# Kernel optimization log

Hardware: AMD Instinct MI355X
Metric: run time of the kernel (lower is better)

## Reference

```python
import jax, jax.numpy as jnp
import numpy as np

V, E, S, B, N = 100000, 300, 1024, 64, 5
H = [512, 256, 128]

def setup_inputs() -> dict:
    key = jax.random.key(0)
    ks = jax.random.split(key, 10)
    x = jax.random.randint(ks[0], (B, S), 0, V, dtype=jnp.int32)
    # lengths must be >= n for valid n-gram counts (original assumes this)
    lengths = jax.random.randint(ks[1], (B,), N, S + 1, dtype=jnp.int32)
    sc = lambda f: 1.0 / np.sqrt(f)
    table = jax.random.normal(ks[2], (V, E), dtype=jnp.float32)
    W_slide = jax.random.uniform(ks[3], (N * E, H[0]), jnp.float32, -sc(N * E), sc(N * E))
    b_slide = jax.random.uniform(ks[4], (H[0],), jnp.float32, -sc(N * E), sc(N * E))
    W1 = jax.random.uniform(ks[5], (H[0], H[1]), jnp.float32, -sc(H[0]), sc(H[0]))
    b1 = jax.random.uniform(ks[6], (H[1],), jnp.float32, -sc(H[0]), sc(H[0]))
    W2 = jax.random.uniform(ks[7], (H[1], H[2]), jnp.float32, -sc(H[1]), sc(H[1]))
    b2 = jax.random.uniform(ks[8], (H[2],), jnp.float32, -sc(H[1]), sc(H[1]))
    return {"x": x, "lengths": lengths, "table": table, "W_slide": W_slide,
            "b_slide": b_slide, "W1": W1, "b1": b1, "W2": W2, "b2": b2}

def reference(x, lengths, table, W_slide, b_slide, W1, b1, W2, b2):
    n = N
    Wn = S - (n - 1)  # number of sliding windows per sequence
    emb = table[x]  # [B, S, E]
    # gather sliding windows: [B, Wn, n, E] -> [B, Wn, n*E]
    idx = jnp.arange(Wn)[:, None] + jnp.arange(n)[None, :]
    win = emb[:, idx].reshape(B, Wn, n * E)
    h = win @ W_slide + b_slide              # [B, Wn, H0]
    h = jax.nn.relu(h @ W1 + b1)             # [B, Wn, H1]
    h = jax.nn.relu(h @ W2 + b2)             # [B, Wn, H2]
    # ragged mean over valid n-gram positions per sample
    valid = (lengths - (n - 1)).astype(h.dtype)           # [B]
    mask = (jnp.arange(Wn)[None, :] < (lengths - (n - 1))[:, None]).astype(h.dtype)
    pooled = jnp.einsum('bwh,bw->bh', h, mask) / valid[:, None]
    return pooled
```

## Files before the change

### kernel.cpp

```cpp
#include <hip/hip_runtime.h>

#define B_N    64
#define S_LEN  1024
#define EMB    300
#define EMB_P  304
#define NGRAM  5
#define WPAD   1024
#define MTOT   (B_N * WPAD)
#define K1P    1536
#define H0     512
#define H1D    256
#define H2D    128
#define NK1    (K1P / 32)
#define NSTEP1 (K1P / 64)

#define GATHER_BLOCKS ((MTOT * 38) / 256)
#define WPREP_THREADS (H0 * K1P + H1D * H0 + H2D * H1D)
#define WPREP_BLOCKS  ((WPREP_THREADS + 255) / 256)

typedef _Float16 half8 __attribute__((ext_vector_type(8)));
typedef float  floatx4 __attribute__((ext_vector_type(4)));

typedef const __attribute__((address_space(1))) void* gptr_t;
typedef __attribute__((address_space(3))) void* sptr_t;

__device__ __forceinline__ void gload16(const void* g, void* s) {
  __builtin_amdgcn_global_load_lds((gptr_t)g, (sptr_t)s, 16, 0, 0);
}

__global__ void prep_kernel(const int* __restrict__ x,
                            const int* __restrict__ lengths,
                            const float* __restrict__ table,
                            _Float16* __restrict__ emb,
                            float* __restrict__ out,
                            const float* __restrict__ Ws,
                            const float* __restrict__ W1,
                            const float* __restrict__ W2,
                            _Float16* __restrict__ Bf1,
                            _Float16* __restrict__ Bf2,
                            _Float16* __restrict__ Bf3,
                            int* __restrict__ meta) {
  __shared__ int sN[64], sP[65], sN6[64], sP6[65];
  const int bid = blockIdx.x;
  if (bid < GATHER_BLOCKS) {
    if (bid < 32) out[bid * 256 + threadIdx.x] = 0.0f;
    int tid = bid * 256 + threadIdx.x;
    int tok = tid / 38;
    int c   = tid - tok * 38;
    int valid = lengths[tok >> 10] - (NGRAM - 1);
    int limit = ((valid + 127) & ~127) + (NGRAM - 1);
    if ((tok & 1023) >= limit) return;
    int e = c << 3;
    const float* row = table + (size_t)x[tok] * EMB + e;
    float4 v0 = *(const float4*)row;
    float4 v1 = make_float4(0.0f, 0.0f, 0.0f, 0.0f);
    if (e + 4 < EMB) v1 = *(const float4*)(row + 4);
    union { half8 h8; _Float16 h[8]; } u;
    u.h[0] = (_Float16)v0.x; u.h[1] = (_Float16)v0.y;
    u.h[2] = (_Float16)v0.z; u.h[3] = (_Float16)v0.w;
    u.h[4] = (_Float16)v1.x; u.h[5] = (_Float16)v1.y;
    u.h[6] = (_Float16)v1.z; u.h[7] = (_Float16)v1.w;
    *(half8*)(emb + (size_t)tok * EMB_P + e) = u.h8;
  } else if (bid < GATHER_BLOCKS + WPREP_BLOCKS) {
    int tid = (bid - GATHER_BLOCKS) * 256 + threadIdx.x;
    const int NS = H0 * K1P;
    const int N1 = H1D * H0;
    const int N2 = H2D * H1D;
    if (tid < NS) {
      int n = tid & 511, k = tid >> 9;
      float v = 0.0f;
      if (k < NGRAM * EMB_P) {
        int tn = k / EMB_P, e = k - tn * EMB_P;
        if (e < EMB) v = Ws[(size_t)(tn * EMB + e) * H0 + n];
      }
      int idx = ((((n >> 4) * NK1 + (k >> 5)) << 6) + (((k >> 3) & 3) << 4) + (n & 15)) * 8 + (k & 7);
      Bf1[idx] = (_Float16)v;
    } else if (tid < NS + N1) {
      int t = tid - NS;
      int n = t & 255, k = t >> 8;
      float v = W1[(size_t)k * H1D + n];
      int idx = ((((n >> 4) * 16 + (k >> 5)) << 6) + (((k >> 3) & 3) << 4) + (n & 15)) * 8 + (k & 7);
      Bf2[idx] = (_Float16)v;
    } else if (tid < NS + N1 + N2) {
      int t = tid - (NS + N1);
      int n = t & 127, k = t >> 7;
      float v = W2[(size_t)k * H2D + n];
      int idx = ((((n >> 4) * 8 + (k >> 5)) << 6) + (((k >> 3) & 3) << 4) + (n & 15)) * 8 + (k & 7);
      Bf3[idx] = (_Float16)v;
    }
  } else {
    int t = threadIdx.x;
    if (t < 64) {
      int valid = lengths[t] - (NGRAM - 1);
      sN[t]  = (valid + 127) >> 7;
      sN6[t] = (valid + 63) >> 6;
    }
    __syncthreads();
    if (t == 0) {
      int s = 0, s6 = 0;
      for (int i = 0; i < 64; i++) {
        sP[i] = s;   s  += sN[i];
        sP6[i] = s6; s6 += sN6[i];
      }
      meta[0] = s; meta[1] = s6;
    }
    __syncthreads();
    if (t < 64) {
      int base = sP[t], n = sN[t];
      for (int i = 0; i < n; i++) meta[8 + base + i] = (t << 3) + i;
      int b6 = sP6[t], n6 = sN6[t];
      for (int i = 0; i < n6; i++) meta[520 + b6 + i] = (t << 4) + i;
    }
  }
}

__global__ __launch_bounds__(256, 2)
void gemm1(const _Float16* __restrict__ A, const _Float16* __restrict__ Bf,
           const float* __restrict__ bias, _Float16* __restrict__ Cf,
           const int* __restrict__ meta, int xcdBase) {
  __shared__ _Float16 sA[2][128 * 64];
  __shared__ _Float16 sB[2][128 * 64];

  const int nLive4 = meta[0] << 2;
  const int xcd = xcdBase + (blockIdx.x & 3), bi = blockIdx.x >> 2;
  const int q = nLive4 >> 3, r = nLive4 & 7;
  if (bi >= q + (xcd < r ? 1 : 0)) return;
  const int L = xcd * q + (xcd < r ? xcd : r) + bi;
  const int mt = meta[8 + (L >> 2)], nt = L & 3;

  const int tid  = threadIdx.x;
  const int wave = tid >> 6, lane = tid & 63;
  const int wr   = wave >> 1, wc = wave & 1;
  const int quad = lane >> 4, l16 = lane & 15;

  const long mBase = (long)mt << 7;
  const int  nBase = nt << 7;

  const int srow0  = (wave << 3) + (lane >> 3);
  const int schunk = lane & 7;
  const _Float16* aG[4];
  int sOffA[4];
#pragma unroll
  for (int p = 0; p < 4; p++) {
    int row = (p << 5) + srow0;
    int c   = schunk ^ (row & 7);
    aG[p]   = A + (mBase + row) * EMB_P + (c << 3);
    sOffA[p] = (row << 6) + (schunk << 3);
  }

  const _Float16* bSrc[4];
  int sOffB[4];
#pragma unroll
  for (int p = 0; p < 4; p++) {
    int idx   = (p << 8) + tid;
    int n16l  = idx >> 7;
    int s     = (idx >> 6) & 1;
    int lane_s = idx & 63;
    bSrc[p]  = Bf + (((size_t)((nBase >> 4) + n16l) * NK1 + s) << 9) + (lane_s << 3);
    sOffB[p] = idx << 3;
  }

  int aOff[2][4];
#pragma unroll
  for (int s = 0; s < 2; s++)
#pragma unroll
    for (int i = 0; i < 4; i++) {
      int rr   = (wr << 6) + (i << 4) + l16;
      int slot = ((s << 2) + quad) ^ (l16 & 7);
      aOff[s][i] = (rr << 6) + (slot << 3);
    }
  int bOff[2][4];
#pragma unroll
  for (int s = 0; s < 2; s++)
#pragma unroll
    for (int j = 0; j < 4; j++)
      bOff[s][j] = (((((wc << 2) + j) << 1) + s) << 9) + (lane << 3);

  floatx4 acc[4][4] = {};

#pragma unroll
  for (int p = 0; p < 4; p++) gload16(aG[p], &sA[0][sOffA[p]]);
#pragma unroll
  for (int p = 0; p < 4; p++) gload16(bSrc[p], &sB[0][sOffB[p]]);

#pragma unroll 2
  for (int kk = 0; kk < NSTEP1; kk++) {
    const int cur = kk & 1;
    __syncthreads();
    if (kk + 1 < NSTEP1) {
      const int koA = (kk + 1) << 6;
      const size_t koB = (size_t)(kk + 1) << 10;
#pragma unroll
      for (int p = 0; p < 4; p++) gload16(aG[p] + koA, &sA[cur ^ 1][sOffA[p]]);
#pragma unroll
      for (int p = 0; p < 4; p++) gload16(bSrc[p] + koB, &sB[cur ^ 1][sOffB[p]]);
    }
#pragma unroll
    for (int s = 0; s < 2; s++) {
      half8 aFr[4], bFr[4];
#pragma unroll
      for (int i = 0; i < 4; i++)
        aFr[i] = *(const half8*)(&sA[cur][aOff[s][i]]);
#pragma unroll
      for (int j = 0; j < 4; j++)
        bFr[j] = *(const half8*)(&sB[cur][bOff[s][j]]);
#pragma unroll
      for (int i = 0; i < 4; i++)
#pragma unroll
        for (int j = 0; j < 4; j++)
          acc[i][j] = __builtin_amdgcn_mfma_f32_16x16x32_f16(aFr[i], bFr[j], acc[i][j], 0, 0, 0);
    }
  }

  __syncthreads();
  _Float16* cs = &sA[0][0];
#pragma unroll
  for (int j = 0; j < 4; j++) {
    int cl = (wc << 6) + (j << 4) + l16;
    float bv = bias[nBase + cl];
    int ksl = cl >> 5;
    int sub_hi = ((cl >> 3) & 3) << 4;
    int c7 = cl & 7;
#pragma unroll
    for (int i = 0; i < 4; i++) {
      int m16l = (wr << 2) + i;
#pragma unroll
      for (int rr = 0; rr < 4; rr++) {
        int ml = (quad << 2) + rr;
        cs[(((m16l << 2) + ksl) << 9) + ((sub_hi + ml) << 3) + c7] =
            (_Float16)(acc[i][j][rr] + bv);
      }
    }
  }
  __syncthreads();
#pragma unroll
  for (int it = 0; it < 8; it++) {
    int cid = (it << 2) + wave;
    int m16l = cid >> 2, ksl = cid & 3;
    size_t g = ((size_t)(((mt << 3) + m16l) * 16 + (nt << 2) + ksl) << 9) + (lane << 3);
    *(half8*)(Cf + g) = *(const half8*)(cs + (cid << 9) + (lane << 3));
  }
}

__global__ __launch_bounds__(256, 3)
void gemm23(const _Float16* __restrict__ Af, const _Float16* __restrict__ B2,
            const _Float16* __restrict__ B3, const float* __restrict__ bias1,
            const float* __restrict__ bias2, float* __restrict__ out,
            const int* __restrict__ lengths, const int* __restrict__ meta) {
  __shared__ _Float16 sH[16384];

  if ((int)blockIdx.x >= meta[1]) return;
  const int mt = meta[520 + blockIdx.x];

  const int tid  = threadIdx.x;
  const int wave = tid >> 6, lane = tid & 63;
  const int wc   = wave;
  const int quad = lane >> 4, l16 = lane & 15;

  const int b = mt >> 4;
  const int validw = lengths[b] - (NGRAM - 1);

  const _Float16* aB = Af + (((size_t)(mt << 2) * 16) << 9) + (lane << 3);
  const _Float16* bB = B2 + ((size_t)wc << 15) + (lane << 3);

  floatx4 acc2[4][4] = {};
  half8 aP[4], bP[4], aQ[4], bQ[4];

  auto loadA = [&](half8* d, int kk) {
#pragma unroll
    for (int i = 0; i < 4; i++)
      d[i] = *(const half8*)(aB + ((size_t)kk << 9) + ((size_t)i << 13));
  };
  auto loadB = [&](half8* d, int kk) {
#pragma unroll
    for (int j = 0; j < 4; j++)
      d[j] = *(const half8*)(bB + ((size_t)kk << 9) + ((size_t)j << 13));
  };
  auto mfmaStep = [&](const half8* aF, const half8* bF) {
    __builtin_amdgcn_s_setprio(1);
#pragma unroll
    for (int i = 0; i < 4; i++)
#pragma unroll
      for (int j = 0; j < 4; j++)
        acc2[i][j] = __builtin_amdgcn_mfma_f32_16x16x32_f16(aF[i], bF[j], acc2[i][j], 0, 0, 0);
    __builtin_amdgcn_s_setprio(0);
  };

  loadA(aP, 0); loadB(bP, 0);
#pragma unroll
  for (int kk = 0; kk < 16; kk += 2) {
    loadA(aQ, kk + 1); loadB(bQ, kk + 1);
    mfmaStep(aP, bP);
    if (kk + 2 < 16) { loadA(aP, kk + 2); loadB(bP, kk + 2); }
    mfmaStep(aQ, bQ);
  }

#pragma unroll
  for (int j = 0; j < 4; j++) {
    int n = (wc << 6) + (j << 4) + l16;
    float bv = bias1[n];
    int ks = n >> 5;
    int sub_hi = ((n >> 3) & 3) << 4;
    int c7 = n & 7;
#pragma unroll
    for (int i = 0; i < 4; i++) {
#pragma unroll
      for (int rr = 0; rr < 4; rr++) {
        int ml = (quad << 2) + rr;
        sH[(((i << 3) + ks) << 9) + ((sub_hi + ml) << 3) + c7] =
            (_Float16)fmaxf(acc2[i][j][rr] + bv, 0.0f);
      }
    }
  }
  __syncthreads();

  const _Float16* b3R[2];
#pragma unroll
  for (int j = 0; j < 2; j++)
    b3R[j] = B3 + (((size_t)((wc << 1) + j) * 8) << 9) + (lane << 3);

  floatx4 acc3[4][2] = {};
#pragma unroll
  for (int ks = 0; ks < 8; ks++) {
    half8 aF[4], bF[2];
#pragma unroll
    for (int i = 0; i < 4; i++)
      aF[i] = *(const half8*)(sH + (((i << 3) + ks) << 9) + (lane << 3));
#pragma unroll
    for (int j = 0; j < 2; j++) bF[j] = *(const half8*)(b3R[j] + ((size_t)ks << 9));
    __builtin_amdgcn_s_setprio(1);
#pragma unroll
    for (int i = 0; i < 4; i++)
#pragma unroll
      for (int j = 0; j < 2; j++)
        acc3[i][j] = __builtin_amdgcn_mfma_f32_16x16x32_f16(aF[i], bF[j], acc3[i][j], 0, 0, 0);
    __builtin_amdgcn_s_setprio(0);
  }

  float inv = 1.0f / (float)validw;
  int wBase = (mt & 15) << 6;
#pragma unroll
  for (int j = 0; j < 2; j++) {
    int col = (wc << 5) + (j << 4) + l16;
    float bv = bias2[col];
    float p = 0.0f;
#pragma unroll
    for (int i = 0; i < 4; i++) {
#pragma unroll
      for (int rr = 0; rr < 4; rr++) {
        int w = wBase + (i << 4) + (quad << 2) + rr;
        float v = fmaxf(acc3[i][j][rr] + bv, 0.0f);
        p += (w < validw) ? v : 0.0f;
      }
    }
    p *= inv;
    p += __shfl_xor(p, 16, 64);
    p += __shfl_xor(p, 32, 64);
    if (quad == 0) atomicAdd(out + b * H2D + col, p);
  }
}

extern "C" void kernel_launch(void* const* d_in, const int* in_sizes, int n_in,
                              void* d_out, int out_size, void* d_ws, size_t ws_size,
                              hipStream_t stream) {
  const int*   x       = (const int*)d_in[0];
  const int*   lengths = (const int*)d_in[1];
  const float* table   = (const float*)d_in[2];
  const float* W_slide = (const float*)d_in[3];
  const float* b_slide = (const float*)d_in[4];
  const float* W1      = (const float*)d_in[5];
  const float* b1      = (const float*)d_in[6];
  const float* W2      = (const float*)d_in[7];
  const float* b2      = (const float*)d_in[8];
  float* out = (float*)d_out;

  _Float16* ws  = (_Float16*)d_ws;
  _Float16* emb = ws;
  _Float16* Bf1 = emb + (size_t)MTOT * EMB_P + 4096;
  _Float16* Bf2 = Bf1 + (size_t)H0 * K1P;
  _Float16* Bf3 = Bf2 + (size_t)H1D * H0;
  _Float16* h1f = Bf3 + (size_t)H2D * H1D;
  int*      meta = (int*)(h1f + (size_t)MTOT * H0);

  prep_kernel<<<GATHER_BLOCKS + WPREP_BLOCKS + 1, 256, 0, stream>>>(
      x, lengths, table, emb, out, W_slide, W1, W2, Bf1, Bf2, Bf3, meta);
  gemm1<<<1024, 256, 0, stream>>>(emb, Bf1, b_slide, h1f, meta, 0);
  gemm1<<<1024, 256, 0, stream>>>(emb, Bf1, b_slide, h1f, meta, 4);
  gemm23<<<MTOT / 64, 256, 0, stream>>>(h1f, Bf2, Bf3, b1, b2, out, lengths, meta);
}
```

Before: 292.9 us.

## Single-buffer gemm1 LDS for higher occupancy and merge two launches into one

Replaces the double-buffered LDS staging in gemm1 with a single 32KB buffer that is loaded and then consumed, with a barrier on each side, and raises launch bounds from 2 to 3 blocks per CU. It also folds the two per-XCD-half launches into one launch of 2048 blocks that maps blockIdx across 8 XCDs. The aim is more resident waves to hide latency and one less launch. The cost is that global loads no longer overlap MFMA compute within a block, so the kernel relies on other resident blocks to hide memory latency.

```diff
diff --git a/kernel.cpp b/kernel.cpp
--- a/kernel.cpp
+++ b/kernel.cpp
@@ -114,15 +114,14 @@
   }
 }
 
-__global__ __launch_bounds__(256, 2)
+__global__ __launch_bounds__(256, 3)
 void gemm1(const _Float16* __restrict__ A, const _Float16* __restrict__ Bf,
            const float* __restrict__ bias, _Float16* __restrict__ Cf,
-           const int* __restrict__ meta, int xcdBase) {
-  __shared__ _Float16 sA[2][128 * 64];
-  __shared__ _Float16 sB[2][128 * 64];
+           const int* __restrict__ meta) {
+  __shared__ _Float16 sm[16384];
 
   const int nLive4 = meta[0] << 2;
-  const int xcd = xcdBase + (blockIdx.x & 3), bi = blockIdx.x >> 2;
+  const int xcd = blockIdx.x & 7, bi = blockIdx.x >> 3;
   const int q = nLive4 >> 3, r = nLive4 & 7;
   if (bi >= q + (xcd < r ? 1 : 0)) return;
   const int L = xcd * q + (xcd < r ? xcd : r) + bi;
@@ -152,12 +151,12 @@
   int sOffB[4];
 #pragma unroll
   for (int p = 0; p < 4; p++) {
-    int idx   = (p << 8) + tid;
-    int n16l  = idx >> 7;
-    int s     = (idx >> 6) & 1;
+    int idx    = (p << 8) + tid;
+    int n16l   = idx >> 7;
+    int s      = (idx >> 6) & 1;
     int lane_s = idx & 63;
     bSrc[p]  = Bf + (((size_t)((nBase >> 4) + n16l) * NK1 + s) << 9) + (lane_s << 3);
-    sOffB[p] = idx << 3;
+    sOffB[p] = 8192 + (idx << 3);
   }
 
   int aOff[2][4];
@@ -174,36 +173,29 @@
   for (int s = 0; s < 2; s++)
 #pragma unroll
     for (int j = 0; j < 4; j++)
-      bOff[s][j] = (((((wc << 2) + j) << 1) + s) << 9) + (lane << 3);
+      bOff[s][j] = 8192 + ((((((wc << 2) + j) << 1) + s) << 9) + (lane << 3));
 
   floatx4 acc[4][4] = {};
-
-#pragma unroll
-  for (int p = 0; p < 4; p++) gload16(aG[p], &sA[0][sOffA[p]]);
-#pragma unroll
-  for (int p = 0; p < 4; p++) gload16(bSrc[p], &sB[0][sOffB[p]]);
 
 #pragma unroll 2
   for (int kk = 0; kk < NSTEP1; kk++) {
-    const int cur = kk & 1;
     __syncthreads();
-    if (kk + 1 < NSTEP1) {
-      const int koA = (kk + 1) << 6;
-      const size_t koB = (size_t)(kk + 1) << 10;
-#pragma unroll
-      for (int p = 0; p < 4; p++) gload16(aG[p] + koA, &sA[cur ^ 1][sOffA[p]]);
-#pragma unroll
-      for (int p = 0; p < 4; p++) gload16(bSrc[p] + koB, &sB[cur ^ 1][sOffB[p]]);
-    }
+    const int koA = kk << 6;
+    const size_t koB = (size_t)kk << 10;
+#pragma unroll
+    for (int p = 0; p < 4; p++) gload16(aG[p] + koA, &sm[sOffA[p]]);
+#pragma unroll
+    for (int p = 0; p < 4; p++) gload16(bSrc[p] + koB, &sm[sOffB[p]]);
+    __syncthreads();
 #pragma unroll
     for (int s = 0; s < 2; s++) {
       half8 aFr[4], bFr[4];
 #pragma unroll
       for (int i = 0; i < 4; i++)
-        aFr[i] = *(const half8*)(&sA[cur][aOff[s][i]]);
+        aFr[i] = *(const half8*)(&sm[aOff[s][i]]);
 #pragma unroll
       for (int j = 0; j < 4; j++)
-        bFr[j] = *(const half8*)(&sB[cur][bOff[s][j]]);
+        bFr[j] = *(const half8*)(&sm[bOff[s][j]]);
 #pragma unroll
       for (int i = 0; i < 4; i++)
 #pragma unroll
@@ -213,7 +205,7 @@
   }
 
   __syncthreads();
-  _Float16* cs = &sA[0][0];
+  _Float16* cs = &sm[0];
 #pragma unroll
   for (int j = 0; j < 4; j++) {
     int cl = (wc << 6) + (j << 4) + l16;
@@ -384,7 +376,6 @@
 
   prep_kernel<<<GATHER_BLOCKS + WPREP_BLOCKS + 1, 256, 0, stream>>>(
       x, lengths, table, emb, out, W_slide, W1, W2, Bf1, Bf2, Bf3, meta);
-  gemm1<<<1024, 256, 0, stream>>>(emb, Bf1, b_slide, h1f, meta, 0);
-  gemm1<<<1024, 256, 0, stream>>>(emb, Bf1, b_slide, h1f, meta, 4);
+  gemm1<<<(MTOT / 128) * (H0 / 128), 256, 0, stream>>>(emb, Bf1, b_slide, h1f, meta);
   gemm23<<<MTOT / 64, 256, 0, stream>>>(h1f, Bf2, Bf3, b1, b2, out, lengths, meta);
 }
```

After: 264.2 us, median of 2. -9.8%, faster.
